# Performance work log

Hardware: AMD Instinct MI355X
Metric: run time of the kernel (lower is better)

The kernel has to match this reference:

```python
import jax, jax.numpy as jnp
import numpy as np

B, S, D = 4, 2048, 1024
H, HD = 16, 64            # num heads, head dim (H*HD == D)
FF = 4096                  # llama intermediate size
EPS = 1e-6
THETA = 10000.0


def rms_norm(x, w):
    v = jnp.mean(jnp.square(x), axis=-1, keepdims=True)
    return x * jax.lax.rsqrt(v + EPS) * w


def apply_rope(x, pos):
    # x: [B,H,S,HD]; HF llama rotate_half convention
    inv = 1.0 / (THETA ** (jnp.arange(0, HD, 2, dtype=jnp.float32) / HD))  # [HD/2]
    ang = pos[:, None].astype(jnp.float32) * inv[None, :]                   # [S,HD/2]
    cos = jnp.concatenate([jnp.cos(ang), jnp.cos(ang)], -1)[None, None]     # [1,1,S,HD]
    sin = jnp.concatenate([jnp.sin(ang), jnp.sin(ang)], -1)[None, None]
    x1, x2 = jnp.split(x, 2, axis=-1)
    return x * cos + jnp.concatenate([-x2, x1], axis=-1) * sin


def setup_inputs() -> dict:
    key = jax.random.key(0)
    ks = jax.random.split(key, 12)
    p = lambda k, shp: (0.02 * jax.random.normal(k, shp, dtype=jnp.float32))
    return {
        "chunk_hidden_states": jax.random.normal(ks[0], (B, S, D), dtype=jnp.float32),
        "Wq": p(ks[1], (D, D)),
        "Wk": p(ks[2], (D, D)),
        "Wv": p(ks[3], (D, D)),
        "Wo": p(ks[4], (D, D)),
        "ln1_w": jnp.ones((D,), dtype=jnp.float32),
        "ln2_w": jnp.ones((D,), dtype=jnp.float32),
        "Wgate": p(ks[5], (FF, D)),
        "Wup": p(ks[6], (FF, D)),
        "Wdown": p(ks[7], (D, FF)),
        "W_out": p(ks[8], (1024, D)),
        "b_out": jnp.zeros((1024,), dtype=jnp.float32),
    }


def reference(chunk_hidden_states, Wq, Wk, Wv, Wo, ln1_w, ln2_w,
              Wgate, Wup, Wdown, W_out, b_out):
    x = chunk_hidden_states                      # [B,S,D]
    pos = jnp.arange(S)

    # --- self attention block ---
    h = rms_norm(x, ln1_w)
    q = (h @ Wq.T).reshape(B, S, H, HD).transpose(0, 2, 1, 3)  # [B,H,S,HD]
    k = (h @ Wk.T).reshape(B, S, H, HD).transpose(0, 2, 1, 3)
    v = (h @ Wv.T).reshape(B, S, H, HD).transpose(0, 2, 1, 3)
    q = apply_rope(q, pos)
    k = apply_rope(k, pos)
    # attention_mask is None when the layer is called directly -> full (non-causal) attention
    scores = jnp.einsum("bhqd,bhkd->bhqk", q, k) / jnp.sqrt(jnp.float32(HD))
    attn = jax.nn.softmax(scores, axis=-1)
    ctx = jnp.einsum("bhqk,bhkd->bhqd", attn, v)             # [B,H,S,HD]
    ctx = ctx.transpose(0, 2, 1, 3).reshape(B, S, D)
    x = x + ctx @ Wo.T

    # --- MLP block (SwiGLU) ---
    h2 = rms_norm(x, ln2_w)
    mlp = (jax.nn.silu(h2 @ Wgate.T) * (h2 @ Wup.T)) @ Wdown.T
    x = x + mlp

    # --- output head ---
    logits = x @ W_out.T + b_out                 # [B,S,1024]
    return logits.reshape(-1, 8, 1024)
```

## Files before the change

### kernel.cpp

```cpp
#include <hip/hip_runtime.h>

#define TB 4
#define TS 2048
#define TD 1024
#define TH 16
#define THD 64
#define TFF 4096
#define TTOK (TB*TS)

typedef unsigned int  uint32;
typedef unsigned short u16;
typedef short s8v __attribute__((ext_vector_type(8)));
typedef short s4bf __attribute__((ext_vector_type(4)));
typedef float f4v __attribute__((ext_vector_type(4)));

#define BF16_MAGIC 0x3f803f80u

__device__ __forceinline__ u16 f2bf(float f){
    uint32 u = __float_as_uint(f);
    u += 0x7fffu + ((u >> 16) & 1u);
    return (u16)(u >> 16);
}
__device__ __forceinline__ float bf2f(u16 h){
    return __uint_as_float(((uint32)h) << 16);
}
__device__ __forceinline__ void gload_lds16(const void* g, void* l){
    __builtin_amdgcn_global_load_lds(
        (const __attribute__((address_space(1))) unsigned int*)g,
        (__attribute__((address_space(3))) unsigned int*)l,
        16, 0, 0);
}

struct CvtDesc { const void* src; void* dst; int n; int mode; };
struct CvtArgs { CvtDesc d[13]; };

__global__ __launch_bounds__(256)
void cvt_all(CvtArgs a, const uint32* __restrict__ flag){
    const bool isbf = (*flag == BF16_MAGIC);
    CvtDesc dd = a.d[blockIdx.y];
    if (dd.mode == 2){
        float* cosT = (float*)dd.dst;
        float* sinT = cosT + TS*32;
        for (int i = blockIdx.x*256 + threadIdx.x; i < dd.n; i += 256*gridDim.x){
            int s = i >> 5, f = i & 31;
            double inv = pow(10000.0, -(double)f/32.0);
            double ang = (double)s * inv;
            cosT[i] = (float)cos(ang);
            sinT[i] = (float)sin(ang);
        }
        return;
    }
    int n4 = dd.n >> 2;
    if (dd.mode == 0){
        u16* dst = (u16*)dd.dst;
        for (int i = blockIdx.x*256 + threadIdx.x; i < n4; i += 256*gridDim.x){
            ushort4 o;
            if (isbf) o = ((const ushort4*)dd.src)[i];
            else {
                float4 v = ((const float4*)dd.src)[i];
                o.x=f2bf(v.x); o.y=f2bf(v.y); o.z=f2bf(v.z); o.w=f2bf(v.w);
            }
            ((ushort4*)dst)[i] = o;
        }
    } else {
        float* dst = (float*)dd.dst;
        for (int i = blockIdx.x*256 + threadIdx.x; i < n4; i += 256*gridDim.x){
            float4 v;
            if (isbf){
                ushort4 u = ((const ushort4*)dd.src)[i];
                v = make_float4(bf2f(u.x), bf2f(u.y), bf2f(u.z), bf2f(u.w));
            } else v = ((const float4*)dd.src)[i];
            ((float4*)dst)[i] = v;
        }
    }
}

__global__ __launch_bounds__(256)
void rmsnorm_k(const float* __restrict__ x, const float* __restrict__ w, u16* __restrict__ out){
    int row = blockIdx.x, tid = threadIdx.x;
    float4 xv = ((const float4*)(x + (size_t)row*TD))[tid];
    float s = xv.x*xv.x + xv.y*xv.y + xv.z*xv.z + xv.w*xv.w;
    #pragma unroll
    for (int off = 32; off > 0; off >>= 1) s += __shfl_xor(s, off);
    __shared__ float red[4];
    if ((tid & 63) == 0) red[tid >> 6] = s;
    __syncthreads();
    float tot = red[0]+red[1]+red[2]+red[3];
    float rs = rsqrtf(tot * (1.0f/TD) + 1e-6f);
    float4 wv = ((const float4*)w)[tid];
    ushort4 o;
    o.x = f2bf(xv.x*rs*wv.x); o.y = f2bf(xv.y*rs*wv.y);
    o.z = f2bf(xv.z*rs*wv.z); o.w = f2bf(xv.w*rs*wv.w);
    ((ushort4*)(out + (size_t)row*TD))[tid] = o;
}

enum { EPI_BF16 = 0, EPI_ADDF32 = 1, EPI_SWIGLU = 2, EPI_OUT = 3, EPI_QKVROPE = 4, EPI_ADDBF16 = 5 };

template<int EPI>
__global__ __launch_bounds__(256)
void gemm_bt(const u16* __restrict__ A, int lda,
             const u16* __restrict__ W, int ldw,
             int K,
             void* __restrict__ outp, int ldo,
             const u16* __restrict__ aux_bf,
             const float* __restrict__ bias,
             const uint32* __restrict__ flag,
             u16* __restrict__ q_out, u16* __restrict__ k_out, u16* __restrict__ v_out,
             const float* __restrict__ cosT, const float* __restrict__ sinT,
             const float* __restrict__ resid)
{
    __shared__ u16 As[128*64];
    __shared__ u16 Bs[128*64];
    const int tid  = threadIdx.x;
    const int wave = tid >> 6;
    const int lane = tid & 63;
    const int tm = blockIdx.y * 128;
    const int tn = blockIdx.x * 128;
    const int wm = (wave >> 1) * 64;
    const int wn = (wave &  1) * 64;

    f4v acc[4][4] = {};

    const int srow8 = lane >> 3;
    const int ch    = lane & 7;
    const int lrow  = lane & 15;
    const int lq    = lane >> 4;

    const u16* Ag = A + (size_t)(tm + wave*32 + srow8)*lda + ((ch ^ srow8) << 3);
    const u16* Wg = W + (size_t)(tn + wave*32 + srow8)*ldw + ((ch ^ srow8) << 3);

    for (int k0 = 0; k0 < K; k0 += 64){
        __syncthreads();
        #pragma unroll
        for (int i8 = 0; i8 < 4; i8++){
            gload_lds16(Ag + (size_t)(i8*8)*lda + k0, As + (wave*32 + i8*8)*64);
            gload_lds16(Wg + (size_t)(i8*8)*ldw + k0, Bs + (wave*32 + i8*8)*64);
        }
        __syncthreads();

        #pragma unroll
        for (int kk = 0; kk < 2; kk++){
            s8v a[4], b[4];
            #pragma unroll
            for (int i = 0; i < 4; i++){
                int row = wm + i*16 + lrow;
                a[i] = *(const s8v*)(As + row*64 + (((kk*4 + lq) ^ (lrow & 7)) << 3));
            }
            #pragma unroll
            for (int j = 0; j < 4; j++){
                int row = wn + j*16 + lrow;
                b[j] = *(const s8v*)(Bs + row*64 + (((kk*4 + lq) ^ (lrow & 7)) << 3));
            }
            #pragma unroll
            for (int i = 0; i < 4; i++)
                #pragma unroll
                for (int j = 0; j < 4; j++)
                    acc[i][j] = __builtin_amdgcn_mfma_f32_16x16x32_bf16(a[i], b[j], acc[i][j], 0, 0, 0);
        }
    }

    if constexpr (EPI == EPI_QKVROPE){
        const int ncol0 = tn + wn;
        if (ncol0 < 2048){
            u16* dst = (ncol0 < 1024) ? q_out : k_out;
            const int cbase = ncol0 & 1023;
            #pragma unroll
            for (int i = 0; i < 4; i++){
                #pragma unroll
                for (int r = 0; r < 4; r++){
                    int row = tm + wm + i*16 + lq*4 + r;
                    int s = row & (TS-1);
                    #pragma unroll
                    for (int j = 0; j < 2; j++){
                        int d = j*16 + lrow;
                        float c  = cosT[s*32 + d];
                        float sn = sinT[s*32 + d];
                        float x1 = acc[i][j][r], x2 = acc[i][j+2][r];
                        dst[(size_t)row*TD + cbase + d]      = f2bf(x1*c - x2*sn);
                        dst[(size_t)row*TD + cbase + d + 32] = f2bf(x2*c + x1*sn);
                    }
                }
            }
        } else {
            #pragma unroll
            for (int i = 0; i < 4; i++)
                #pragma unroll
                for (int j = 0; j < 4; j++)
                    #pragma unroll
                    for (int r = 0; r < 4; r++){
                        int row = tm + wm + i*16 + lq*4 + r;
                        int col = ncol0 - 2048 + j*16 + lrow;
                        v_out[(size_t)row*TD + col] = f2bf(acc[i][j][r]);
                    }
        }
        return;
    }

    bool obf = false;
    if (EPI == EPI_OUT) obf = (*flag == BF16_MAGIC);
    #pragma unroll
    for (int i = 0; i < 4; i++){
        #pragma unroll
        for (int j = 0; j < 4; j++){
            #pragma unroll
            for (int r = 0; r < 4; r++){
                int row = tm + wm + i*16 + lq*4 + r;
                int col = tn + wn + j*16 + lrow;
                size_t idx = (size_t)row*ldo + col;
                float val = acc[i][j][r];
                if constexpr (EPI == EPI_BF16){
                    ((u16*)outp)[idx] = f2bf(val);
                } else if constexpr (EPI == EPI_ADDF32){
                    float* o = (float*)outp;
                    o[idx] += val;
                } else if constexpr (EPI == EPI_SWIGLU){
                    float g = bf2f(aux_bf[idx]);
                    float mres = (g / (1.0f + __expf(-g))) * val;
                    ((u16*)outp)[idx] = f2bf(mres);
                } else if constexpr (EPI == EPI_ADDBF16){
                    ((u16*)outp)[idx] = f2bf(resid[idx] + val);
                } else {
                    float v2 = val + bias[col];
                    if (obf) ((u16*)outp)[idx] = f2bf(v2);
                    else     ((float*)outp)[idx] = v2;
                }
            }
        }
    }
}

__global__ __launch_bounds__(256, 2)
void flash_attn_mfma(const u16* __restrict__ qg, const u16* __restrict__ kg,
                     const u16* __restrict__ vg, u16* __restrict__ ctx)
{
    __shared__ u16 Qs[128*64];
    __shared__ u16 Ks[64*64];
    __shared__ u16 VT[64*66];
    const int tid  = threadIdx.x;
    const int wave = tid >> 6;
    const int lane = tid & 63;
    const int qd   = lane >> 4;
    const int mm   = lane & 15;
    const int b  = blockIdx.y >> 4, h = blockIdx.y & 15;
    const int q0 = blockIdx.x * 128;
    const size_t tok0 = (size_t)b * TS;
    const int rl = lane >> 3, ch = lane & 7;

    #pragma unroll
    for (int i = 0; i < 4; i++){
        int row = wave*32 + i*8 + rl;
        const u16* gp = qg + (tok0 + q0 + row)*TD + h*THD + ((ch ^ (row & 7)) << 3);
        gload_lds16(gp, Qs + (wave*32 + i*8)*64);
    }
    __syncthreads();

    s8v qf[2][2];
    #pragma unroll
    for (int ct = 0; ct < 2; ct++){
        int row = wave*32 + ct*16 + mm;
        #pragma unroll
        for (int hs = 0; hs < 2; hs++)
            qf[ct][hs] = *(const s8v*)(Qs + row*64 + (((hs*4 + qd) ^ (row & 7)) << 3));
    }

    f4v acc[2][4] = {};
    float mrun[2] = {-3.0e38f, -3.0e38f};
    float lrun[2] = {0.0f, 0.0f};
    const float SC2 = 0.18033688011112042f;

    for (int kt = 0; kt < TS/64; kt++){
        __syncthreads();
        #pragma unroll
        for (int i = 0; i < 2; i++){
            int row = wave*16 + i*8 + rl;
            const u16* gp = kg + (tok0 + kt*64 + row)*TD + h*THD + ((ch ^ (row & 7)) << 3);
            gload_lds16(gp, Ks + (wave*16 + i*8)*64);
        }
        {
            int vk = tid >> 4, h4 = tid & 15;
            #pragma unroll
            for (int i = 0; i < 4; i++){
                int key = vk + i*16;
                ushort4 vv = *(const ushort4*)(vg + (tok0 + kt*64 + key)*TD + h*THD + h4*4);
                VT[(h4*4+0)*66 + key] = vv.x;
                VT[(h4*4+1)*66 + key] = vv.y;
                VT[(h4*4+2)*66 + key] = vv.z;
                VT[(h4*4+3)*66 + key] = vv.w;
            }
        }
        __syncthreads();

        f4v sc[4][2] = {};
        #pragma unroll
        for (int rt = 0; rt < 4; rt++){
            int row = rt*16 + mm;
            #pragma unroll
            for (int hs = 0; hs < 2; hs++){
                s8v kf = *(const s8v*)(Ks + row*64 + (((hs*4 + qd) ^ (row & 7)) << 3));
                #pragma unroll
                for (int ct = 0; ct < 2; ct++)
                    sc[rt][ct] = __builtin_amdgcn_mfma_f32_16x16x32_bf16(kf, qf[ct][hs], sc[rt][ct], 0, 0, 0);
            }
        }
        s4bf vf[4][4];
        #pragma unroll
        for (int rt = 0; rt < 4; rt++)
            #pragma unroll
            for (int n = 0; n < 4; n++)
                vf[rt][n] = *(const s4bf*)(&VT[(16*n + mm)*66 + rt*16 + qd*4]);

        #pragma unroll
        for (int ct = 0; ct < 2; ct++){
            float mx = sc[0][ct][0];
            #pragma unroll
            for (int rt = 0; rt < 4; rt++)
                #pragma unroll
                for (int r = 0; r < 4; r++)
                    mx = fmaxf(mx, sc[rt][ct][r]);
            mx = fmaxf(mx, __shfl_xor(mx, 16));
            mx = fmaxf(mx, __shfl_xor(mx, 32));
            float mn = fmaxf(mrun[ct], mx * SC2);
            float alpha = __builtin_amdgcn_exp2f(mrun[ct] - mn);
            mrun[ct] = mn;
            float ls = 0.0f;
            uint32 pk[4][2];
            #pragma unroll
            for (int rt = 0; rt < 4; rt++){
                float p0 = __builtin_amdgcn_exp2f(fmaf(sc[rt][ct][0], SC2, -mn));
                float p1 = __builtin_amdgcn_exp2f(fmaf(sc[rt][ct][1], SC2, -mn));
                float p2 = __builtin_amdgcn_exp2f(fmaf(sc[rt][ct][2], SC2, -mn));
                float p3 = __builtin_amdgcn_exp2f(fmaf(sc[rt][ct][3], SC2, -mn));
                ls += (p0 + p1) + (p2 + p3);
                pk[rt][0] = (__float_as_uint(p0) >> 16) | (__float_as_uint(p1) & 0xFFFF0000u);
                pk[rt][1] = (__float_as_uint(p2) >> 16) | (__float_as_uint(p3) & 0xFFFF0000u);
            }
            ls += __shfl_xor(ls, 16);
            ls += __shfl_xor(ls, 32);
            lrun[ct] = lrun[ct]*alpha + ls;
            #pragma unroll
            for (int r = 0; r < 4; r++){
                float ar = __shfl(alpha, (lane & 48) + qd*4 + r);
                #pragma unroll
                for (int n = 0; n < 4; n++)
                    acc[ct][n][r] *= ar;
            }
            #pragma unroll
            for (int rt = 0; rt < 4; rt++){
                union { uint32 u[2]; s4bf s; } pu;
                pu.u[0] = pk[rt][0]; pu.u[1] = pk[rt][1];
                #pragma unroll
                for (int n = 0; n < 4; n++)
                    acc[ct][n] = __builtin_amdgcn_mfma_f32_16x16x16bf16_1k(pu.s, vf[rt][n], acc[ct][n], 0, 0, 0);
            }
        }
    }
    #pragma unroll
    for (int ct = 0; ct < 2; ct++){
        float rli = 1.0f / lrun[ct];
        #pragma unroll
        for (int r = 0; r < 4; r++){
            float ir = __shfl(rli, (lane & 48) + qd*4 + r);
            int row = q0 + wave*32 + ct*16 + qd*4 + r;
            u16* op = ctx + (tok0 + row)*TD + h*THD + mm;
            #pragma unroll
            for (int n = 0; n < 4; n++)
                op[16*n] = f2bf(acc[ct][n][r] * ir);
        }
    }
}

extern "C" void kernel_launch(void* const* d_in, const int* in_sizes, int n_in,
                              void* d_out, int out_size, void* d_ws, size_t ws_size,
                              hipStream_t stream)
{
    const uint32* flag = (const uint32*)d_in[5];
    char* ws = (char*)d_ws;
    size_t off = 0;
    auto alloc = [&](size_t bytes) -> void* {
        void* p = ws + off;
        off += (bytes + 255) & ~(size_t)255;
        return p;
    };
    float* xf   = (float*)alloc((size_t)TTOK*TD*4);
    u16*   hbf  = (u16*)  alloc((size_t)TTOK*TD*2);
    u16*   qb   = (u16*)  alloc((size_t)TTOK*TD*2);
    u16*   kb   = (u16*)  alloc((size_t)TTOK*TD*2);
    u16*   vb   = (u16*)  alloc((size_t)TTOK*TD*2);
    u16*   cb   = (u16*)  alloc((size_t)TTOK*TD*2);
    u16*   wqkv = (u16*)  alloc((size_t)3*TD*TD*2);
    u16*   wo   = (u16*)  alloc((size_t)TD*TD*2);
    u16*   wg   = (u16*)  alloc((size_t)TFF*TD*2);
    u16*   wu   = (u16*)  alloc((size_t)TFF*TD*2);
    u16*   wd   = (u16*)  alloc((size_t)TD*TFF*2);
    u16*   wou  = (u16*)  alloc((size_t)TD*TD*2);
    float* ln1  = (float*)alloc(TD*4);
    float* ln2  = (float*)alloc(TD*4);
    float* bo   = (float*)alloc(TD*4);
    float* cosT = (float*)alloc((size_t)TS*32*4*2);
    float* sinT = cosT + TS*32;
    u16*   gbuf = qb;
    (void)ws_size; (void)in_sizes; (void)n_in; (void)out_size;

    CvtArgs ca;
    ca.d[0]  = { d_in[0],  xf,            TTOK*TD, 1 };
    ca.d[1]  = { d_in[1],  wqkv,          TD*TD,   0 };
    ca.d[2]  = { d_in[2],  wqkv + (size_t)TD*TD,   TD*TD, 0 };
    ca.d[3]  = { d_in[3],  wqkv + (size_t)2*TD*TD, TD*TD, 0 };
    ca.d[4]  = { d_in[4],  wo,            TD*TD,   0 };
    ca.d[5]  = { d_in[7],  wg,            TFF*TD,  0 };
    ca.d[6]  = { d_in[8],  wu,            TFF*TD,  0 };
    ca.d[7]  = { d_in[9],  wd,            TD*TFF,  0 };
    ca.d[8]  = { d_in[10], wou,           TD*TD,   0 };
    ca.d[9]  = { d_in[5],  ln1,           TD,      1 };
    ca.d[10] = { d_in[6],  ln2,           TD,      1 };
    ca.d[11] = { d_in[11], bo,            TD,      1 };
    ca.d[12] = { nullptr,  cosT,          TS*32,   2 };
    cvt_all<<<dim3(256,13),256,0,stream>>>(ca, flag);

    rmsnorm_k<<<TTOK,256,0,stream>>>(xf, ln1, hbf);
    gemm_bt<EPI_QKVROPE><<<dim3(24, TTOK/128),256,0,stream>>>(
        hbf, TD, wqkv, TD, TD, nullptr, 0, nullptr, nullptr, nullptr,
        qb, kb, vb, cosT, sinT, nullptr);
    flash_attn_mfma<<<dim3(TS/128, TB*TH),256,0,stream>>>(qb, kb, vb, cb);
    gemm_bt<EPI_ADDF32><<<dim3(TD/128, TTOK/128),256,0,stream>>>(
        cb, TD, wo, TD, TD, xf, TD, nullptr, nullptr, nullptr,
        nullptr, nullptr, nullptr, nullptr, nullptr, nullptr);

    rmsnorm_k<<<TTOK,256,0,stream>>>(xf, ln2, hbf);
    gemm_bt<EPI_BF16><<<dim3(TFF/128, TTOK/128),256,0,stream>>>(
        hbf, TD, wg, TD, TD, gbuf, TFF, nullptr, nullptr, nullptr,
        nullptr, nullptr, nullptr, nullptr, nullptr, nullptr);
    gemm_bt<EPI_SWIGLU><<<dim3(TFF/128, TTOK/128),256,0,stream>>>(
        hbf, TD, wu, TD, TD, gbuf, TFF, gbuf, nullptr, nullptr,
        nullptr, nullptr, nullptr, nullptr, nullptr, nullptr);
    gemm_bt<EPI_ADDBF16><<<dim3(TD/128, TTOK/128),256,0,stream>>>(
        gbuf, TFF, wd, TFF, TFF, hbf, TD, nullptr, nullptr, nullptr,
        nullptr, nullptr, nullptr, nullptr, nullptr, xf);

    gemm_bt<EPI_OUT><<<dim3(TD/128, TTOK/128),256,0,stream>>>(
        hbf, TD, wou, TD, TD, d_out, TD, nullptr, bo, flag,
        nullptr, nullptr, nullptr, nullptr, nullptr, nullptr);
}
```

Baseline: 719.0 us.

## Fuse gate/up GEMMs with SwiGLU epilogue and store V pre-transposed for attention

The gate and up weights are interleaved per 64-row block into one matrix, so a single GEMM computes gate and up tiles side by side and applies SwiGLU through an LDS exchange. This drops the intermediate gate buffer write and re-read and one kernel launch. The QKV GEMM now writes V transposed per head, so attention can load it with direct LDS copies instead of a scalar transpose, and the PV product moves from 16x16x16 to 16x16x32 MFMA. The costs are strided scalar stores of transposed V in the QKV epilogue and an extra LDS round trip in the fused MLP epilogue.

```diff
diff --git a/kernel.cpp b/kernel.cpp
--- a/kernel.cpp
+++ b/kernel.cpp
@@ -51,18 +51,7 @@
         return;
     }
     int n4 = dd.n >> 2;
-    if (dd.mode == 0){
-        u16* dst = (u16*)dd.dst;
-        for (int i = blockIdx.x*256 + threadIdx.x; i < n4; i += 256*gridDim.x){
-            ushort4 o;
-            if (isbf) o = ((const ushort4*)dd.src)[i];
-            else {
-                float4 v = ((const float4*)dd.src)[i];
-                o.x=f2bf(v.x); o.y=f2bf(v.y); o.z=f2bf(v.z); o.w=f2bf(v.w);
-            }
-            ((ushort4*)dst)[i] = o;
-        }
-    } else {
+    if (dd.mode == 1){
         float* dst = (float*)dd.dst;
         for (int i = blockIdx.x*256 + threadIdx.x; i < n4; i += 256*gridDim.x){
             float4 v;
@@ -72,6 +61,22 @@
             } else v = ((const float4*)dd.src)[i];
             ((float4*)dst)[i] = v;
         }
+        return;
+    }
+    for (int i = blockIdx.x*256 + threadIdx.x; i < n4; i += 256*gridDim.x){
+        ushort4 o;
+        if (isbf) o = ((const ushort4*)dd.src)[i];
+        else {
+            float4 v = ((const float4*)dd.src)[i];
+            o.x=f2bf(v.x); o.y=f2bf(v.y); o.z=f2bf(v.z); o.w=f2bf(v.w);
+        }
+        size_t di = i;
+        if (dd.mode >= 3){
+            int row = i >> 8, c4 = i & 255;
+            int drow = ((row >> 6) << 7) + (row & 63) + ((dd.mode == 4) ? 64 : 0);
+            di = (size_t)drow*256 + c4;
+        }
+        ((ushort4*)dd.dst)[di] = o;
     }
 }
 
@@ -94,7 +99,7 @@
     ((ushort4*)(out + (size_t)row*TD))[tid] = o;
 }
 
-enum { EPI_BF16 = 0, EPI_ADDF32 = 1, EPI_SWIGLU = 2, EPI_OUT = 3, EPI_QKVROPE = 4, EPI_ADDBF16 = 5 };
+enum { EPI_ADDF32 = 1, EPI_OUT = 3, EPI_QKVROPE = 4, EPI_ADDBF16 = 5, EPI_GATEUP = 6 };
 
 template<int EPI>
 __global__ __launch_bounds__(256)
@@ -102,15 +107,15 @@
              const u16* __restrict__ W, int ldw,
              int K,
              void* __restrict__ outp, int ldo,
-             const u16* __restrict__ aux_bf,
              const float* __restrict__ bias,
              const uint32* __restrict__ flag,
-             u16* __restrict__ q_out, u16* __restrict__ k_out, u16* __restrict__ v_out,
+             u16* __restrict__ q_out, u16* __restrict__ k_out, u16* __restrict__ vt_out,
              const float* __restrict__ cosT, const float* __restrict__ sinT,
              const float* __restrict__ resid)
 {
-    __shared__ u16 As[128*64];
-    __shared__ u16 Bs[128*64];
+    __shared__ __align__(16) u16 SMEM[2*128*64];
+    u16* As = SMEM;
+    u16* Bs = SMEM + 128*64;
     const int tid  = threadIdx.x;
     const int wave = tid >> 6;
     const int lane = tid & 63;
@@ -190,7 +195,41 @@
                     for (int r = 0; r < 4; r++){
                         int row = tm + wm + i*16 + lq*4 + r;
                         int col = ncol0 - 2048 + j*16 + lrow;
-                        v_out[(size_t)row*TD + col] = f2bf(acc[i][j][r]);
+                        int bb = row >> 11, s = row & (TS-1);
+                        int hh = col >> 6, hd = col & 63;
+                        vt_out[((size_t)(bb*TH + hh)*THD + hd)*TS + s] = f2bf(acc[i][j][r]);
+                    }
+        }
+        return;
+    }
+
+    if constexpr (EPI == EPI_GATEUP){
+        __syncthreads();
+        float* upL = (float*)SMEM;
+        const int widx = wave >> 1;
+        if (wave & 1){
+            #pragma unroll
+            for (int i = 0; i < 4; i++)
+                #pragma unroll
+                for (int j = 0; j < 4; j++)
+                    #pragma unroll
+                    for (int r = 0; r < 4; r++)
+                        upL[widx*4096 + (i*16 + lq*4 + r)*64 + j*16 + lrow] = acc[i][j][r];
+        }
+        __syncthreads();
+        if (!(wave & 1)){
+            #pragma unroll
+            for (int i = 0; i < 4; i++)
+                #pragma unroll
+                for (int j = 0; j < 4; j++)
+                    #pragma unroll
+                    for (int r = 0; r < 4; r++){
+                        float g = acc[i][j][r];
+                        float u = upL[widx*4096 + (i*16 + lq*4 + r)*64 + j*16 + lrow];
+                        float mres = (g / (1.0f + __expf(-g))) * u;
+                        int row = tm + wm + i*16 + lq*4 + r;
+                        int fcol = blockIdx.x*64 + j*16 + lrow;
+                        ((u16*)outp)[(size_t)row*TFF + fcol] = f2bf(mres);
                     }
         }
         return;
@@ -208,15 +247,9 @@
                 int col = tn + wn + j*16 + lrow;
                 size_t idx = (size_t)row*ldo + col;
                 float val = acc[i][j][r];
-                if constexpr (EPI == EPI_BF16){
-                    ((u16*)outp)[idx] = f2bf(val);
-                } else if constexpr (EPI == EPI_ADDF32){
+                if constexpr (EPI == EPI_ADDF32){
                     float* o = (float*)outp;
                     o[idx] += val;
-                } else if constexpr (EPI == EPI_SWIGLU){
-                    float g = bf2f(aux_bf[idx]);
-                    float mres = (g / (1.0f + __expf(-g))) * val;
-                    ((u16*)outp)[idx] = f2bf(mres);
                 } else if constexpr (EPI == EPI_ADDBF16){
                     ((u16*)outp)[idx] = f2bf(resid[idx] + val);
                 } else {
@@ -231,11 +264,11 @@
 
 __global__ __launch_bounds__(256, 2)
 void flash_attn_mfma(const u16* __restrict__ qg, const u16* __restrict__ kg,
-                     const u16* __restrict__ vg, u16* __restrict__ ctx)
+                     const u16* __restrict__ vt, u16* __restrict__ ctx)
 {
     __shared__ u16 Qs[128*64];
     __shared__ u16 Ks[64*64];
-    __shared__ u16 VT[64*66];
+    __shared__ u16 VT2[8*64*8];
     const int tid  = threadIdx.x;
     const int wave = tid >> 6;
     const int lane = tid & 63;
@@ -244,6 +277,7 @@
     const int b  = blockIdx.y >> 4, h = blockIdx.y & 15;
     const int q0 = blockIdx.x * 128;
     const size_t tok0 = (size_t)b * TS;
+    const u16* vtb = vt + (size_t)(b*TH + h)*THD*TS;
     const int rl = lane >> 3, ch = lane & 7;
 
     #pragma unroll
@@ -276,17 +310,11 @@
             const u16* gp = kg + (tok0 + kt*64 + row)*TD + h*THD + ((ch ^ (row & 7)) << 3);
             gload_lds16(gp, Ks + (wave*16 + i*8)*64);
         }
-        {
-            int vk = tid >> 4, h4 = tid & 15;
-            #pragma unroll
-            for (int i = 0; i < 4; i++){
-                int key = vk + i*16;
-                ushort4 vv = *(const ushort4*)(vg + (tok0 + kt*64 + key)*TD + h*THD + h4*4);
-                VT[(h4*4+0)*66 + key] = vv.x;
-                VT[(h4*4+1)*66 + key] = vv.y;
-                VT[(h4*4+2)*66 + key] = vv.z;
-                VT[(h4*4+3)*66 + key] = vv.w;
-            }
+        #pragma unroll
+        for (int ii = 0; ii < 2; ii++){
+            int kb = wave*2 + ii;
+            const u16* gp = vtb + (size_t)lane*TS + kt*64 + kb*8;
+            gload_lds16(gp, VT2 + kb*64*8);
         }
         __syncthreads();
 
@@ -302,12 +330,18 @@
                     sc[rt][ct] = __builtin_amdgcn_mfma_f32_16x16x32_bf16(kf, qf[ct][hs], sc[rt][ct], 0, 0, 0);
             }
         }
-        s4bf vf[4][4];
-        #pragma unroll
-        for (int rt = 0; rt < 4; rt++)
-            #pragma unroll
-            for (int n = 0; n < 4; n++)
-                vf[rt][n] = *(const s4bf*)(&VT[(16*n + mm)*66 + rt*16 + qd*4]);
+        union VU { s4bf h[2]; s8v v; };
+        VU vf8[2][4];
+        #pragma unroll
+        for (int t = 0; t < 2; t++){
+            int kbA = 4*t + (qd >> 1);
+            #pragma unroll
+            for (int n = 0; n < 4; n++){
+                const u16* base = VT2 + ((16*n + mm)*8) + ((qd & 1) * 4);
+                vf8[t][n].h[0] = *(const s4bf*)(base + kbA*512);
+                vf8[t][n].h[1] = *(const s4bf*)(base + (kbA+2)*512);
+            }
+        }
 
         #pragma unroll
         for (int ct = 0; ct < 2; ct++){
@@ -345,12 +379,13 @@
                     acc[ct][n][r] *= ar;
             }
             #pragma unroll
-            for (int rt = 0; rt < 4; rt++){
-                union { uint32 u[2]; s4bf s; } pu;
-                pu.u[0] = pk[rt][0]; pu.u[1] = pk[rt][1];
+            for (int t = 0; t < 2; t++){
+                union { uint32 u[4]; s8v s; } pu;
+                pu.u[0] = pk[2*t][0];   pu.u[1] = pk[2*t][1];
+                pu.u[2] = pk[2*t+1][0]; pu.u[3] = pk[2*t+1][1];
                 #pragma unroll
                 for (int n = 0; n < 4; n++)
-                    acc[ct][n] = __builtin_amdgcn_mfma_f32_16x16x16bf16_1k(pu.s, vf[rt][n], acc[ct][n], 0, 0, 0);
+                    acc[ct][n] = __builtin_amdgcn_mfma_f32_16x16x32_bf16(pu.s, vf8[t][n].v, acc[ct][n], 0, 0, 0);
             }
         }
     }
@@ -385,12 +420,11 @@
     u16*   hbf  = (u16*)  alloc((size_t)TTOK*TD*2);
     u16*   qb   = (u16*)  alloc((size_t)TTOK*TD*2);
     u16*   kb   = (u16*)  alloc((size_t)TTOK*TD*2);
-    u16*   vb   = (u16*)  alloc((size_t)TTOK*TD*2);
     u16*   cb   = (u16*)  alloc((size_t)TTOK*TD*2);
+    u16*   vt   = (u16*)  alloc((size_t)TTOK*TD*2);
     u16*   wqkv = (u16*)  alloc((size_t)3*TD*TD*2);
     u16*   wo   = (u16*)  alloc((size_t)TD*TD*2);
-    u16*   wg   = (u16*)  alloc((size_t)TFF*TD*2);
-    u16*   wu   = (u16*)  alloc((size_t)TFF*TD*2);
+    u16*   wfu  = (u16*)  alloc((size_t)2*TFF*TD*2);
     u16*   wd   = (u16*)  alloc((size_t)TD*TFF*2);
     u16*   wou  = (u16*)  alloc((size_t)TD*TD*2);
     float* ln1  = (float*)alloc(TD*4);
@@ -398,7 +432,7 @@
     float* bo   = (float*)alloc(TD*4);
     float* cosT = (float*)alloc((size_t)TS*32*4*2);
     float* sinT = cosT + TS*32;
-    u16*   gbuf = qb;
+    u16*   mbuf = qb;
     (void)ws_size; (void)in_sizes; (void)n_in; (void)out_size;
 
     CvtArgs ca;
@@ -407,8 +441,8 @@
     ca.d[2]  = { d_in[2],  wqkv + (size_t)TD*TD,   TD*TD, 0 };
     ca.d[3]  = { d_in[3],  wqkv + (size_t)2*TD*TD, TD*TD, 0 };
     ca.d[4]  = { d_in[4],  wo,            TD*TD,   0 };
-    ca.d[5]  = { d_in[7],  wg,            TFF*TD,  0 };
-    ca.d[6]  = { d_in[8],  wu,            TFF*TD,  0 };
+    ca.d[5]  = { d_in[7],  wfu,           TFF*TD,  3 };
+    ca.d[6]  = { d_in[8],  wfu,           TFF*TD,  4 };
     ca.d[7]  = { d_in[9],  wd,            TD*TFF,  0 };
     ca.d[8]  = { d_in[10], wou,           TD*TD,   0 };
     ca.d[9]  = { d_in[5],  ln1,           TD,      1 };
@@ -419,25 +453,22 @@
 
     rmsnorm_k<<<TTOK,256,0,stream>>>(xf, ln1, hbf);
     gemm_bt<EPI_QKVROPE><<<dim3(24, TTOK/128),256,0,stream>>>(
-        hbf, TD, wqkv, TD, TD, nullptr, 0, nullptr, nullptr, nullptr,
-        qb, kb, vb, cosT, sinT, nullptr);
-    flash_attn_mfma<<<dim3(TS/128, TB*TH),256,0,stream>>>(qb, kb, vb, cb);
+        hbf, TD, wqkv, TD, TD, nullptr, 0, nullptr, nullptr,
+        qb, kb, vt, cosT, sinT, nullptr);
+    flash_attn_mfma<<<dim3(TS/128, TB*TH),256,0,stream>>>(qb, kb, vt, cb);
     gemm_bt<EPI_ADDF32><<<dim3(TD/128, TTOK/128),256,0,stream>>>(
-        cb, TD, wo, TD, TD, xf, TD, nullptr, nullptr, nullptr,
+        cb, TD, wo, TD, TD, xf, TD, nullptr, nullptr,
         nullptr, nullptr, nullptr, nullptr, nullptr, nullptr);
 
     rmsnorm_k<<<TTOK,256,0,stream>>>(xf, ln2, hbf);
-    gemm_bt<EPI_BF16><<<dim3(TFF/128, TTOK/128),256,0,stream>>>(
-        hbf, TD, wg, TD, TD, gbuf, TFF, nullptr, nullptr, nullptr,
-        nullptr, nullptr, nullptr, nullptr, nullptr, nullptr);
-    gemm_bt<EPI_SWIGLU><<<dim3(TFF/128, TTOK/128),256,0,stream>>>(
-        hbf, TD, wu, TD, TD, gbuf, TFF, gbuf, nullptr, nullptr,
+    gemm_bt<EPI_GATEUP><<<dim3(2*TFF/128, TTOK/128),256,0,stream>>>(
+        hbf, TD, wfu, TD, TD, mbuf, TFF, nullptr, nullptr,
         nullptr, nullptr, nullptr, nullptr, nullptr, nullptr);
     gemm_bt<EPI_ADDBF16><<<dim3(TD/128, TTOK/128),256,0,stream>>>(
-        gbuf, TFF, wd, TFF, TFF, hbf, TD, nullptr, nullptr, nullptr,
+        mbuf, TFF, wd, TFF, TFF, hbf, TD, nullptr, nullptr,
         nullptr, nullptr, nullptr, nullptr, nullptr, xf);
 
     gemm_bt<EPI_OUT><<<dim3(TD/128, TTOK/128),256,0,stream>>>(
-        hbf, TD, wou, TD, TD, d_out, TD, nullptr, bo, flag,
+        hbf, TD, wou, TD, TD, d_out, TD, bo, flag,
         nullptr, nullptr, nullptr, nullptr, nullptr, nullptr);
 }
```

Measured after the change: 699.9 us. 2.7% less time.
